# Optimization experiments

Measured on AMD Instinct MI355X. Metric: run time of the kernel, lower is better.

The kernel has to match this reference:

```python
import jax, jax.numpy as jnp
import numpy as np

N = 100000   # n_nodes
E = 600000   # n_edges
D = 128      # cfg_node_encoding_dim
L = 4        # nr_layers
EPS = 1e-5


def setup_inputs() -> dict:
    key = jax.random.key(0)
    k0, k1, k2, k3 = jax.random.split(key, 4)
    x = jax.random.normal(k0, (N, D), dtype=jnp.float32)
    edge_index = jax.random.randint(k1, (2, E), 0, N, dtype=jnp.int32)
    W = jax.random.normal(k2, (L, D, D), dtype=jnp.float32) * (1.0 / np.sqrt(D))
    b = jax.random.normal(k3, (L, D), dtype=jnp.float32) * 0.01
    gamma = jnp.ones((L, D), dtype=jnp.float32)
    beta = jnp.zeros((L, D), dtype=jnp.float32)
    return {"x": x, "W": W, "b": b, "gamma": gamma, "beta": beta,
            "edge_index": edge_index}


def _gcn_layer(x, W, b, src_sl, dst_sl, norm):
    # PyG GCNConv: h = x @ W, then symmetric-normalized aggregation + bias
    h = x @ W                                  # [N, D]
    msg = h[src_sl] * norm[:, None]            # [E+N, D] gather + scale
    out = jax.ops.segment_sum(msg, dst_sl, num_segments=N)  # scatter-add
    return out + b


def _layer_norm(x, gamma, beta):
    mu = jnp.mean(x, axis=-1, keepdims=True)
    var = jnp.mean(jnp.square(x - mu), axis=-1, keepdims=True)
    return (x - mu) * jax.lax.rsqrt(var + EPS) * gamma + beta


def reference(x, W, b, gamma, beta, edge_index):
    src, dst = edge_index[0], edge_index[1]
    loops = jnp.arange(N, dtype=edge_index.dtype)
    src_sl = jnp.concatenate([src, loops])     # add_self_loops=True
    dst_sl = jnp.concatenate([dst, loops])
    deg = jax.ops.segment_sum(jnp.ones(E + N, dtype=x.dtype), dst_sl,
                              num_segments=N)
    dinv = jnp.where(deg > 0, jax.lax.rsqrt(deg), 0.0)
    norm = dinv[src_sl] * dinv[dst_sl]         # D^{-1/2} (A+I) D^{-1/2}
    h = x
    for i in range(L):
        h = _gcn_layer(h, W[i], b[i], src_sl, dst_sl, norm)
        h = jax.nn.relu(h)
        # dropout is identity in eval mode
        h = _layer_norm(h, gamma[i], beta[i])
    return h
```

## Files before the change

### kernel.cpp

```cpp
#include <hip/hip_runtime.h>
#include <hip/hip_bf16.h>

#define D_DIM 128
#define AST 136

typedef __attribute__((ext_vector_type(8))) short short8v;
typedef __attribute__((ext_vector_type(4))) short short4v;
typedef __attribute__((ext_vector_type(4))) float floatx4;

__device__ __forceinline__ short f2bf(float x) {
    unsigned u = __builtin_bit_cast(unsigned, x);
    unsigned r = u + 0x7fff + ((u >> 16) & 1);
    return (short)(r >> 16);
}
__device__ __forceinline__ float bflo(unsigned p) {
    return __builtin_bit_cast(float, p << 16);
}
__device__ __forceinline__ float bfhi(unsigned p) {
    return __builtin_bit_cast(float, p & 0xffff0000u);
}


__global__ void zero_cnt_kernel(int* __restrict__ cnt, int n) {
    int i = blockIdx.x * blockDim.x + threadIdx.x;
    if (i < n) cnt[i] = 0;
}

__global__ void count_kernel(const int* __restrict__ dst, int* __restrict__ cnt, int e) {
    int i = blockIdx.x * blockDim.x + threadIdx.x;
    if (i < e) atomicAdd(&cnt[dst[i]], 1);
}

__global__ __launch_bounds__(256) void partial_kernel(const int* __restrict__ cnt,
                                                      int* __restrict__ partial, int n) {
    const int b = blockIdx.x, t = threadIdx.x;
    const int base = b * 1024 + t * 4;
    int s = 0;
    if (base + 3 < n) {
        int4 c = *(const int4*)(cnt + base);
        s = c.x + c.y + c.z + c.w;
    } else {
        for (int j = 0; j < 4; ++j) if (base + j < n) s += cnt[base + j];
    }
    #pragma unroll
    for (int m = 1; m < 64; m <<= 1) s += __shfl_xor(s, m, 64);
    __shared__ int ws[4];
    if ((t & 63) == 0) ws[t >> 6] = s;
    __syncthreads();
    if (t == 0) partial[b] = ws[0] + ws[1] + ws[2] + ws[3];
}

__global__ __launch_bounds__(1024) void scan_partials_kernel(int* __restrict__ partial, int nb,
                                                             int* __restrict__ row_ptr,
                                                             int n, int e) {
    __shared__ int sh[1024];
    const int t = threadIdx.x;
    sh[t] = (t < nb) ? partial[t] : 0;
    __syncthreads();
    for (int off = 1; off < 1024; off <<= 1) {
        int v = (t >= off) ? sh[t - off] : 0;
        __syncthreads();
        sh[t] += v;
        __syncthreads();
    }
    if (t < nb) partial[t] = (t == 0) ? 0 : sh[t - 1];
    if (t == 0) row_ptr[n] = e;
}

__global__ __launch_bounds__(256) void emit_kernel(const int* __restrict__ cnt,
                                                   const int* __restrict__ partial,
                                                   int* __restrict__ row_ptr,
                                                   int* __restrict__ cursor,
                                                   float* __restrict__ dinv, int n) {
    const int b = blockIdx.x, t = threadIdx.x;
    const int base = b * 1024 + t * 4;
    int4 c = make_int4(0, 0, 0, 0);
    if (base + 3 < n) {
        c = *(const int4*)(cnt + base);
    } else {
        if (base     < n) c.x = cnt[base];
        if (base + 1 < n) c.y = cnt[base + 1];
        if (base + 2 < n) c.z = cnt[base + 2];
        if (base + 3 < n) c.w = cnt[base + 3];
    }
    const int ts = c.x + c.y + c.z + c.w;
    int incl = ts;
    const int lane = t & 63;
    #pragma unroll
    for (int off = 1; off < 64; off <<= 1) {
        int v = __shfl_up(incl, off, 64);
        if (lane >= off) incl += v;
    }
    __shared__ int wsum[4];
    if (lane == 63) wsum[t >> 6] = incl;
    __syncthreads();
    const int w = t >> 6;
    int waveoff = 0;
    #pragma unroll
    for (int i = 0; i < 3; ++i) if (i < w) waveoff += wsum[i];
    const int basev = partial[b] + waveoff + (incl - ts);
    const int e0 = basev, e1 = e0 + c.x, e2 = e1 + c.y, e3 = e2 + c.z;
    if (base + 3 < n) {
        *(int4*)(row_ptr + base) = make_int4(e0, e1, e2, e3);
        *(int4*)(cursor  + base) = make_int4(e0, e1, e2, e3);
        *(float4*)(dinv + base) = make_float4(rsqrtf((float)(c.x + 1)), rsqrtf((float)(c.y + 1)),
                                              rsqrtf((float)(c.z + 1)), rsqrtf((float)(c.w + 1)));
    } else {
        int es[4] = {e0, e1, e2, e3};
        int cs[4] = {c.x, c.y, c.z, c.w};
        for (int j = 0; j < 4; ++j) if (base + j < n) {
            row_ptr[base + j] = es[j];
            cursor[base + j]  = es[j];
            dinv[base + j]    = rsqrtf((float)(cs[j] + 1));
        }
    }
}

__global__ void fill_kernel(const int* __restrict__ src, const int* __restrict__ dst,
                            const float* __restrict__ dinv,
                            int* __restrict__ cursor, int2* __restrict__ meta, int e) {
    int i = blockIdx.x * blockDim.x + threadIdx.x;
    if (i < e) {
        int s = src[i], d = dst[i];
        int p = atomicAdd(&cursor[d], 1);
        float w = dinv[s] * dinv[d];
        meta[p] = make_int2(s, __builtin_bit_cast(int, w));
    }
}

__global__ __launch_bounds__(256) void wt_prep_kernel(const float* __restrict__ W,
                                                      short* __restrict__ Wt, int total) {
    int o = blockIdx.x * blockDim.x + threadIdx.x;
    if (o >= total) return;
    int l = o >> 14;
    int r = o & 16383;
    int nn = r >> 7;
    int k  = r & 127;
    Wt[o] = f2bf(W[(size_t)l * 16384 + (size_t)k * 128 + nn]);
}

template <bool IN_F32>
__global__ __launch_bounds__(256) void gemm_mfma_kernel(const void* __restrict__ Xv,
                                                        const short* __restrict__ Wt,
                                                        short* __restrict__ H, int n) {
    __shared__ short Alds[64 * AST];
    __shared__ short Wlds[128 * AST];
    const int t = threadIdx.x;
    const int row0 = blockIdx.x * 64;

    #pragma unroll
    for (int i = 0; i < 8; ++i) {
        int q  = t + i * 256;
        int nn = q >> 4;
        int kc = q & 15;
        short8v v = *(const short8v*)(Wt + nn * 128 + kc * 8);
        *(short8v*)(&Wlds[nn * AST + kc * 8]) = v;
    }
    if constexpr (IN_F32) {
        const float* X = (const float*)Xv;
        #pragma unroll
        for (int i = 0; i < 8; ++i) {
            int q  = t + i * 256;
            int r  = q >> 5;
            int k4 = q & 31;
            int row = row0 + r;
            float4 v = make_float4(0.f, 0.f, 0.f, 0.f);
            if (row < n) v = *(const float4*)(X + (size_t)row * D_DIM + k4 * 4);
            short4v s;
            s.x = f2bf(v.x); s.y = f2bf(v.y); s.z = f2bf(v.z); s.w = f2bf(v.w);
            *(short4v*)(&Alds[r * AST + k4 * 4]) = s;
        }
    } else {
        const short* X = (const short*)Xv;
        #pragma unroll
        for (int i = 0; i < 4; ++i) {
            int q  = t + i * 256;
            int r  = q >> 4;
            int kc = q & 15;
            int row = row0 + r;
            short8v v = {0,0,0,0,0,0,0,0};
            if (row < n) v = *(const short8v*)(X + (size_t)row * D_DIM + kc * 8);
            *(short8v*)(&Alds[r * AST + kc * 8]) = v;
        }
    }
    __syncthreads();

    const int wv   = t >> 6;
    const int lane = t & 63;
    const int m    = lane & 15;
    const int quad = lane >> 4;

    const short* abase = &Alds[(wv * 16 + m) * AST + quad * 8];
    const short* bbase = &Wlds[m * AST + quad * 8];

    short8v afr[4];
    #pragma unroll
    for (int kt = 0; kt < 4; ++kt) afr[kt] = *(const short8v*)(abase + kt * 32);

    floatx4 acc[8];
    #pragma unroll
    for (int c = 0; c < 8; ++c) acc[c] = (floatx4){0.f, 0.f, 0.f, 0.f};

    #pragma unroll
    for (int c = 0; c < 8; ++c) {
        #pragma unroll
        for (int kt = 0; kt < 4; ++kt) {
            short8v bfr = *(const short8v*)(bbase + c * 16 * AST + kt * 32);
            acc[c] = __builtin_amdgcn_mfma_f32_16x16x32_bf16(afr[kt], bfr, acc[c], 0, 0, 0);
        }
    }

    #pragma unroll
    for (int c = 0; c < 8; ++c) {
        #pragma unroll
        for (int r = 0; r < 4; ++r) {
            int row = row0 + wv * 16 + quad * 4 + r;
            if (row < n) H[(size_t)row * D_DIM + c * 16 + m] = f2bf(acc[c][r]);
        }
    }
}

template <bool OUT_BF16>
__global__ __launch_bounds__(256) void agg_kernel(const short* __restrict__ Hb,
                                                  const int* __restrict__ row_ptr,
                                                  const int2* __restrict__ meta,
                                                  const float* __restrict__ dinv,
                                                  const float* __restrict__ bias,
                                                  const float* __restrict__ gamma,
                                                  const float* __restrict__ beta,
                                                  void* __restrict__ Yv, int n) {
    const int wave = __builtin_amdgcn_readfirstlane(threadIdx.x >> 6);
    const int lane = threadIdx.x & 63;
    const int v = blockIdx.x * 4 + wave;
    if (v >= n) return;

    const float dv = dinv[v];
    const int beg = row_ptr[v];
    const int end = row_ptr[v + 1];

    const unsigned ps = ((const unsigned*)(Hb + (size_t)v * D_DIM))[lane];
    const float wself = dv * dv;
    float ax = bflo(ps) * wself;
    float ay = bfhi(ps) * wself;

    int i = beg;
    for (; i + 4 <= end; i += 4) {
        const int2 m0 = meta[i];
        const int2 m1 = meta[i + 1];
        const int2 m2 = meta[i + 2];
        const int2 m3 = meta[i + 3];
        const unsigned p0 = ((const unsigned*)(Hb + (size_t)m0.x * D_DIM))[lane];
        const unsigned p1 = ((const unsigned*)(Hb + (size_t)m1.x * D_DIM))[lane];
        const unsigned p2 = ((const unsigned*)(Hb + (size_t)m2.x * D_DIM))[lane];
        const unsigned p3 = ((const unsigned*)(Hb + (size_t)m3.x * D_DIM))[lane];
        const float w0 = __builtin_bit_cast(float, m0.y);
        const float w1 = __builtin_bit_cast(float, m1.y);
        const float w2 = __builtin_bit_cast(float, m2.y);
        const float w3 = __builtin_bit_cast(float, m3.y);
        ax = fmaf(w0, bflo(p0), ax);  ay = fmaf(w0, bfhi(p0), ay);
        ax = fmaf(w1, bflo(p1), ax);  ay = fmaf(w1, bfhi(p1), ay);
        ax = fmaf(w2, bflo(p2), ax);  ay = fmaf(w2, bfhi(p2), ay);
        ax = fmaf(w3, bflo(p3), ax);  ay = fmaf(w3, bfhi(p3), ay);
    }
    for (; i < end; ++i) {
        const int2 m0 = meta[i];
        const unsigned p0 = ((const unsigned*)(Hb + (size_t)m0.x * D_DIM))[lane];
        const float w0 = __builtin_bit_cast(float, m0.y);
        ax = fmaf(w0, bflo(p0), ax);
        ay = fmaf(w0, bfhi(p0), ay);
    }

    const float2 bb = ((const float2*)bias)[lane];
    float a0 = fmaxf(ax + bb.x, 0.f);
    float a1 = fmaxf(ay + bb.y, 0.f);

    float s1 = a0 + a1;
    float s2 = a0 * a0 + a1 * a1;
    #pragma unroll
    for (int m = 1; m < 64; m <<= 1) {
        s1 += __shfl_xor(s1, m, 64);
        s2 += __shfl_xor(s2, m, 64);
    }
    const float mu  = s1 * (1.f / 128.f);
    const float var = s2 * (1.f / 128.f) - mu * mu;
    const float rs  = rsqrtf(var + 1e-5f);

    const float2 gg = ((const float2*)gamma)[lane];
    const float2 be = ((const float2*)beta)[lane];
    const float o0 = (a0 - mu) * rs * gg.x + be.x;
    const float o1 = (a1 - mu) * rs * gg.y + be.y;

    if constexpr (OUT_BF16) {
        unsigned pack = (unsigned)(unsigned short)f2bf(o0) |
                        ((unsigned)(unsigned short)f2bf(o1) << 16);
        ((unsigned*)((short*)Yv + (size_t)v * D_DIM))[lane] = pack;
    } else {
        float2 o; o.x = o0; o.y = o1;
        ((float2*)((float*)Yv + (size_t)v * D_DIM))[lane] = o;
    }
}


extern "C" void kernel_launch(void* const* d_in, const int* in_sizes, int n_in,
                              void* d_out, int out_size, void* d_ws, size_t ws_size,
                              hipStream_t stream) {
    const float* x     = (const float*)d_in[0];
    const float* W     = (const float*)d_in[1];
    const float* bias  = (const float*)d_in[2];
    const float* gamma = (const float*)d_in[3];
    const float* beta  = (const float*)d_in[4];
    const int*   edges = (const int*)d_in[5];

    const int N = in_sizes[0] / D_DIM;
    const int E = in_sizes[5] / 2;
    const int L = in_sizes[1] / (D_DIM * D_DIM);

    const int* src = edges;
    const int* dst = edges + E;

    const int NB = (N + 1023) / 1024;

    char* w = (char*)d_ws;
    short* Hb   = (short*)w; w += (size_t)N * D_DIM * sizeof(short);
    short* Act  = (short*)w; w += (size_t)N * D_DIM * sizeof(short);
    int* cnt     = (int*)w;  w += (size_t)((N + 3) & ~3) * sizeof(int);
    int* row_ptr = (int*)w;  w += (size_t)((N + 4) & ~3) * sizeof(int);
    int* cursor  = (int*)w;  w += (size_t)((N + 3) & ~3) * sizeof(int);
    int2* meta   = (int2*)w; w += (size_t)E * sizeof(int2);
    float* dinv  = (float*)w; w += (size_t)((N + 3) & ~3) * sizeof(float);
    int* partial = (int*)w;  w += (size_t)((NB + 3) & ~3) * sizeof(int);
    short* Wt    = (short*)w; w += (size_t)L * D_DIM * D_DIM * sizeof(short);

    zero_cnt_kernel<<<(N + 255) / 256, 256, 0, stream>>>(cnt, N);
    count_kernel<<<(E + 255) / 256, 256, 0, stream>>>(dst, cnt, E);
    partial_kernel<<<NB, 256, 0, stream>>>(cnt, partial, N);
    scan_partials_kernel<<<1, 1024, 0, stream>>>(partial, NB, row_ptr, N, E);
    emit_kernel<<<NB, 256, 0, stream>>>(cnt, partial, row_ptr, cursor, dinv, N);
    fill_kernel<<<(E + 255) / 256, 256, 0, stream>>>(src, dst, dinv, cursor, meta, E);

    const int WT_TOTAL = L * D_DIM * D_DIM;
    wt_prep_kernel<<<(WT_TOTAL + 255) / 256, 256, 0, stream>>>(W, Wt, WT_TOTAL);

    const int GB = (N + 63) / 64;
    const int AB = (N + 3) / 4;

    gemm_mfma_kernel<true><<<GB, 256, 0, stream>>>(x, Wt, Hb, N);
    agg_kernel<true><<<AB, 256, 0, stream>>>(Hb, row_ptr, meta, dinv,
                                             bias, gamma, beta, Act, N);
    for (int l = 1; l < L - 1; ++l) {
        gemm_mfma_kernel<false><<<GB, 256, 0, stream>>>(Act, Wt + (size_t)l * D_DIM * D_DIM, Hb, N);
        agg_kernel<true><<<AB, 256, 0, stream>>>(Hb, row_ptr, meta, dinv,
                                                 bias + (size_t)l * D_DIM,
                                                 gamma + (size_t)l * D_DIM,
                                                 beta + (size_t)l * D_DIM, Act, N);
    }
    {
        int l = L - 1;
        gemm_mfma_kernel<false><<<GB, 256, 0, stream>>>(Act, Wt + (size_t)l * D_DIM * D_DIM, Hb, N);
        agg_kernel<false><<<AB, 256, 0, stream>>>(Hb, row_ptr, meta, dinv,
                                                  bias + (size_t)l * D_DIM,
                                                  gamma + (size_t)l * D_DIM,
                                                  beta + (size_t)l * D_DIM, d_out, N);
    }
}
```

Measured before the change: 394.9 us.

## Drop LDS staging in GEMM and pad aggregation tail to 4-wide batches

The GEMM kernel no longer stages X and W through shared memory. Each wave keeps its own 32 output columns of W in registers, loads A fragments directly from global memory for each of four 16-row tiles, and runs MFMA without a block barrier, trading LDS traffic and sync for redundant global loads of A across waves. The aggregation kernel replaces its scalar remainder loop with a clamped, zero-weighted 4-wide tail, so all neighbor gathers issue in groups of four. The tail iterations fetch redundant rows.

```diff
diff --git a/kernel.cpp b/kernel.cpp
--- a/kernel.cpp
+++ b/kernel.cpp
@@ -2,7 +2,6 @@
 #include <hip/hip_bf16.h>
 
 #define D_DIM 128
-#define AST 136
 
 typedef __attribute__((ext_vector_type(8))) short short8v;
 typedef __attribute__((ext_vector_type(4))) short short4v;
@@ -143,79 +142,58 @@
 __global__ __launch_bounds__(256) void gemm_mfma_kernel(const void* __restrict__ Xv,
                                                         const short* __restrict__ Wt,
                                                         short* __restrict__ H, int n) {
-    __shared__ short Alds[64 * AST];
-    __shared__ short Wlds[128 * AST];
-    const int t = threadIdx.x;
-    const int row0 = blockIdx.x * 64;
-
-    #pragma unroll
-    for (int i = 0; i < 8; ++i) {
-        int q  = t + i * 256;
-        int nn = q >> 4;
-        int kc = q & 15;
-        short8v v = *(const short8v*)(Wt + nn * 128 + kc * 8);
-        *(short8v*)(&Wlds[nn * AST + kc * 8]) = v;
-    }
-    if constexpr (IN_F32) {
-        const float* X = (const float*)Xv;
-        #pragma unroll
-        for (int i = 0; i < 8; ++i) {
-            int q  = t + i * 256;
-            int r  = q >> 5;
-            int k4 = q & 31;
-            int row = row0 + r;
-            float4 v = make_float4(0.f, 0.f, 0.f, 0.f);
-            if (row < n) v = *(const float4*)(X + (size_t)row * D_DIM + k4 * 4);
-            short4v s;
-            s.x = f2bf(v.x); s.y = f2bf(v.y); s.z = f2bf(v.z); s.w = f2bf(v.w);
-            *(short4v*)(&Alds[r * AST + k4 * 4]) = s;
-        }
-    } else {
-        const short* X = (const short*)Xv;
-        #pragma unroll
-        for (int i = 0; i < 4; ++i) {
-            int q  = t + i * 256;
-            int r  = q >> 4;
-            int kc = q & 15;
-            int row = row0 + r;
-            short8v v = {0,0,0,0,0,0,0,0};
-            if (row < n) v = *(const short8v*)(X + (size_t)row * D_DIM + kc * 8);
-            *(short8v*)(&Alds[r * AST + kc * 8]) = v;
-        }
-    }
-    __syncthreads();
-
+    const int t    = threadIdx.x;
     const int wv   = t >> 6;
     const int lane = t & 63;
     const int m    = lane & 15;
     const int quad = lane >> 4;
-
-    const short* abase = &Alds[(wv * 16 + m) * AST + quad * 8];
-    const short* bbase = &Wlds[m * AST + quad * 8];
-
-    short8v afr[4];
-    #pragma unroll
-    for (int kt = 0; kt < 4; ++kt) afr[kt] = *(const short8v*)(abase + kt * 32);
-
-    floatx4 acc[8];
-    #pragma unroll
-    for (int c = 0; c < 8; ++c) acc[c] = (floatx4){0.f, 0.f, 0.f, 0.f};
-
-    #pragma unroll
-    for (int c = 0; c < 8; ++c) {
+    const int row0 = blockIdx.x * 64;
+
+    short8v bfr[2][4];
+    #pragma unroll
+    for (int c = 0; c < 2; ++c) {
+        const short* bp = Wt + (size_t)((wv * 2 + c) * 16 + m) * D_DIM + quad * 8;
         #pragma unroll
-        for (int kt = 0; kt < 4; ++kt) {
-            short8v bfr = *(const short8v*)(bbase + c * 16 * AST + kt * 32);
-            acc[c] = __builtin_amdgcn_mfma_f32_16x16x32_bf16(afr[kt], bfr, acc[c], 0, 0, 0);
+        for (int kt = 0; kt < 4; ++kt)
+            bfr[c][kt] = *(const short8v*)(bp + kt * 32);
+    }
+
+    #pragma unroll
+    for (int rt = 0; rt < 4; ++rt) {
+        const int arow  = row0 + rt * 16 + m;
+        const int arowc = arow < n ? arow : n - 1;
+
+        short8v afr[4];
+        if constexpr (IN_F32) {
+            const float* xp = (const float*)Xv + (size_t)arowc * D_DIM + quad * 8;
+            #pragma unroll
+            for (int kt = 0; kt < 4; ++kt) {
+                float4 v0 = *(const float4*)(xp + kt * 32);
+                float4 v1 = *(const float4*)(xp + kt * 32 + 4);
+                short8v a;
+                a[0] = f2bf(v0.x); a[1] = f2bf(v0.y); a[2] = f2bf(v0.z); a[3] = f2bf(v0.w);
+                a[4] = f2bf(v1.x); a[5] = f2bf(v1.y); a[6] = f2bf(v1.z); a[7] = f2bf(v1.w);
+                afr[kt] = a;
+            }
+        } else {
+            const short* xp = (const short*)Xv + (size_t)arowc * D_DIM + quad * 8;
+            #pragma unroll
+            for (int kt = 0; kt < 4; ++kt)
+                afr[kt] = *(const short8v*)(xp + kt * 32);
         }
-    }
-
-    #pragma unroll
-    for (int c = 0; c < 8; ++c) {
+
         #pragma unroll
-        for (int r = 0; r < 4; ++r) {
-            int row = row0 + wv * 16 + quad * 4 + r;
-            if (row < n) H[(size_t)row * D_DIM + c * 16 + m] = f2bf(acc[c][r]);
+        for (int c = 0; c < 2; ++c) {
+            floatx4 acc = (floatx4){0.f, 0.f, 0.f, 0.f};
+            #pragma unroll
+            for (int kt = 0; kt < 4; ++kt)
+                acc = __builtin_amdgcn_mfma_f32_16x16x32_bf16(afr[kt], bfr[c][kt], acc, 0, 0, 0);
+            const int col = (wv * 2 + c) * 16 + m;
+            #pragma unroll
+            for (int r = 0; r < 4; ++r) {
+                const int row = row0 + rt * 16 + quad * 4 + r;
+                if (row < n) H[(size_t)row * D_DIM + col] = f2bf(acc[r]);
+            }
         }
     }
 }
@@ -243,31 +221,26 @@
     float ax = bflo(ps) * wself;
     float ay = bfhi(ps) * wself;
 
-    int i = beg;
-    for (; i + 4 <= end; i += 4) {
+    for (int i = beg; i < end; i += 4) {
+        const int i1 = min(i + 1, end - 1);
+        const int i2 = min(i + 2, end - 1);
+        const int i3 = min(i + 3, end - 1);
         const int2 m0 = meta[i];
-        const int2 m1 = meta[i + 1];
-        const int2 m2 = meta[i + 2];
-        const int2 m3 = meta[i + 3];
+        const int2 m1 = meta[i1];
+        const int2 m2 = meta[i2];
+        const int2 m3 = meta[i3];
         const unsigned p0 = ((const unsigned*)(Hb + (size_t)m0.x * D_DIM))[lane];
         const unsigned p1 = ((const unsigned*)(Hb + (size_t)m1.x * D_DIM))[lane];
         const unsigned p2 = ((const unsigned*)(Hb + (size_t)m2.x * D_DIM))[lane];
         const unsigned p3 = ((const unsigned*)(Hb + (size_t)m3.x * D_DIM))[lane];
         const float w0 = __builtin_bit_cast(float, m0.y);
-        const float w1 = __builtin_bit_cast(float, m1.y);
-        const float w2 = __builtin_bit_cast(float, m2.y);
-        const float w3 = __builtin_bit_cast(float, m3.y);
+        const float w1 = (i + 1 < end) ? __builtin_bit_cast(float, m1.y) : 0.f;
+        const float w2 = (i + 2 < end) ? __builtin_bit_cast(float, m2.y) : 0.f;
+        const float w3 = (i + 3 < end) ? __builtin_bit_cast(float, m3.y) : 0.f;
         ax = fmaf(w0, bflo(p0), ax);  ay = fmaf(w0, bfhi(p0), ay);
         ax = fmaf(w1, bflo(p1), ax);  ay = fmaf(w1, bfhi(p1), ay);
         ax = fmaf(w2, bflo(p2), ax);  ay = fmaf(w2, bfhi(p2), ay);
         ax = fmaf(w3, bflo(p3), ax);  ay = fmaf(w3, bfhi(p3), ay);
-    }
-    for (; i < end; ++i) {
-        const int2 m0 = meta[i];
-        const unsigned p0 = ((const unsigned*)(Hb + (size_t)m0.x * D_DIM))[lane];
-        const float w0 = __builtin_bit_cast(float, m0.y);
-        ax = fmaf(w0, bflo(p0), ax);
-        ay = fmaf(w0, bfhi(p0), ay);
     }
 
     const float2 bb = ((const float2*)bias)[lane];
```

Result: slower. 424.3 us (+7.5%).

## Keep W fragments in registers and batch 8 neighbor gathers per iteration

Applied to the files above, without the earlier changes.

The GEMM kernel no longer stages the 128x128 bf16 weight tile in LDS. Each wave now loads its two 16-column weight fragments directly into registers and loops over the four 16-row A tiles. This drops the large Wlds allocation and the LDS weight reads, which should raise occupancy, but every block still reads W from global or L2. The aggregation loop now processes 8 neighbors per iteration with clamped indices and zeroed weights for the tail, issuing 8 independent gathers to expose more memory-level parallelism. The cost is redundant loads on the padded tail entries.

```diff
diff --git a/kernel.cpp b/kernel.cpp
--- a/kernel.cpp
+++ b/kernel.cpp
@@ -144,18 +144,22 @@
                                                         const short* __restrict__ Wt,
                                                         short* __restrict__ H, int n) {
     __shared__ short Alds[64 * AST];
-    __shared__ short Wlds[128 * AST];
-    const int t = threadIdx.x;
+    const int t    = threadIdx.x;
+    const int wv   = t >> 6;
+    const int lane = t & 63;
+    const int m    = lane & 15;
+    const int quad = lane >> 4;
     const int row0 = blockIdx.x * 64;
 
-    #pragma unroll
-    for (int i = 0; i < 8; ++i) {
-        int q  = t + i * 256;
-        int nn = q >> 4;
-        int kc = q & 15;
-        short8v v = *(const short8v*)(Wt + nn * 128 + kc * 8);
-        *(short8v*)(&Wlds[nn * AST + kc * 8]) = v;
-    }
+    short8v bfr[2][4];
+    #pragma unroll
+    for (int c = 0; c < 2; ++c) {
+        const short* bp = Wt + (size_t)((wv * 2 + c) * 16 + m) * D_DIM + quad * 8;
+        #pragma unroll
+        for (int kt = 0; kt < 4; ++kt)
+            bfr[c][kt] = *(const short8v*)(bp + kt * 32);
+    }
+
     if constexpr (IN_F32) {
         const float* X = (const float*)Xv;
         #pragma unroll
@@ -185,37 +189,25 @@
     }
     __syncthreads();
 
-    const int wv   = t >> 6;
-    const int lane = t & 63;
-    const int m    = lane & 15;
-    const int quad = lane >> 4;
-
-    const short* abase = &Alds[(wv * 16 + m) * AST + quad * 8];
-    const short* bbase = &Wlds[m * AST + quad * 8];
-
-    short8v afr[4];
-    #pragma unroll
-    for (int kt = 0; kt < 4; ++kt) afr[kt] = *(const short8v*)(abase + kt * 32);
-
-    floatx4 acc[8];
-    #pragma unroll
-    for (int c = 0; c < 8; ++c) acc[c] = (floatx4){0.f, 0.f, 0.f, 0.f};
-
-    #pragma unroll
-    for (int c = 0; c < 8; ++c) {
-        #pragma unroll
-        for (int kt = 0; kt < 4; ++kt) {
-            short8v bfr = *(const short8v*)(bbase + c * 16 * AST + kt * 32);
-            acc[c] = __builtin_amdgcn_mfma_f32_16x16x32_bf16(afr[kt], bfr, acc[c], 0, 0, 0);
-        }
-    }
-
-    #pragma unroll
-    for (int c = 0; c < 8; ++c) {
-        #pragma unroll
-        for (int r = 0; r < 4; ++r) {
-            int row = row0 + wv * 16 + quad * 4 + r;
-            if (row < n) H[(size_t)row * D_DIM + c * 16 + m] = f2bf(acc[c][r]);
+    #pragma unroll
+    for (int rt = 0; rt < 4; ++rt) {
+        const short* ab = &Alds[(rt * 16 + m) * AST + quad * 8];
+        short8v afr[4];
+        #pragma unroll
+        for (int kt = 0; kt < 4; ++kt) afr[kt] = *(const short8v*)(ab + kt * 32);
+
+        #pragma unroll
+        for (int c = 0; c < 2; ++c) {
+            floatx4 acc = (floatx4){0.f, 0.f, 0.f, 0.f};
+            #pragma unroll
+            for (int kt = 0; kt < 4; ++kt)
+                acc = __builtin_amdgcn_mfma_f32_16x16x32_bf16(afr[kt], bfr[c][kt], acc, 0, 0, 0);
+            const int col = (wv * 2 + c) * 16 + m;
+            #pragma unroll
+            for (int r = 0; r < 4; ++r) {
+                const int row = row0 + rt * 16 + quad * 4 + r;
+                if (row < n) H[(size_t)row * D_DIM + col] = f2bf(acc[r]);
+            }
         }
     }
 }
@@ -243,31 +235,25 @@
     float ax = bflo(ps) * wself;
     float ay = bfhi(ps) * wself;
 
-    int i = beg;
-    for (; i + 4 <= end; i += 4) {
-        const int2 m0 = meta[i];
-        const int2 m1 = meta[i + 1];
-        const int2 m2 = meta[i + 2];
-        const int2 m3 = meta[i + 3];
-        const unsigned p0 = ((const unsigned*)(Hb + (size_t)m0.x * D_DIM))[lane];
-        const unsigned p1 = ((const unsigned*)(Hb + (size_t)m1.x * D_DIM))[lane];
-        const unsigned p2 = ((const unsigned*)(Hb + (size_t)m2.x * D_DIM))[lane];
-        const unsigned p3 = ((const unsigned*)(Hb + (size_t)m3.x * D_DIM))[lane];
-        const float w0 = __builtin_bit_cast(float, m0.y);
-        const float w1 = __builtin_bit_cast(float, m1.y);
-        const float w2 = __builtin_bit_cast(float, m2.y);
-        const float w3 = __builtin_bit_cast(float, m3.y);
-        ax = fmaf(w0, bflo(p0), ax);  ay = fmaf(w0, bfhi(p0), ay);
-        ax = fmaf(w1, bflo(p1), ax);  ay = fmaf(w1, bfhi(p1), ay);
-        ax = fmaf(w2, bflo(p2), ax);  ay = fmaf(w2, bfhi(p2), ay);
-        ax = fmaf(w3, bflo(p3), ax);  ay = fmaf(w3, bfhi(p3), ay);
-    }
-    for (; i < end; ++i) {
-        const int2 m0 = meta[i];
-        const unsigned p0 = ((const unsigned*)(Hb + (size_t)m0.x * D_DIM))[lane];
-        const float w0 = __builtin_bit_cast(float, m0.y);
-        ax = fmaf(w0, bflo(p0), ax);
-        ay = fmaf(w0, bfhi(p0), ay);
+    for (int i = beg; i < end; i += 8) {
+        int   idx[8];
+        float wgt[8];
+        #pragma unroll
+        for (int j = 0; j < 8; ++j) {
+            const int ii = min(i + j, end - 1);
+            const int2 mm = meta[ii];
+            idx[j] = mm.x;
+            wgt[j] = (i + j < end) ? __builtin_bit_cast(float, mm.y) : 0.f;
+        }
+        unsigned p[8];
+        #pragma unroll
+        for (int j = 0; j < 8; ++j)
+            p[j] = ((const unsigned*)(Hb + (size_t)idx[j] * D_DIM))[lane];
+        #pragma unroll
+        for (int j = 0; j < 8; ++j) {
+            ax = fmaf(wgt[j], bflo(p[j]), ax);
+            ay = fmaf(wgt[j], bfhi(p[j]), ay);
+        }
     }
 
     const float2 bb = ((const float2*)bias)[lane];
```

Result: faster. 381.8 us (-3.3%).
